# Kernel tuning notes

Hardware: AMD Instinct MI355X
Metric: run time of the kernel (lower is better)

The kernel has to match this reference:

```python
import jax, jax.numpy as jnp
import numpy as np

B, S, D, H, K = 16, 4096, 256, 512, 3
EPS = 1e-5


def setup_inputs() -> dict:
    key = jax.random.key(0)
    ks = jax.random.split(key, 16)
    glorot = lambda k, shape: jax.random.uniform(
        k, shape, jnp.float32, -1.0, 1.0) * np.sqrt(6.0 / (shape[0] + shape[-1]))
    return {
        "inputs": jax.random.normal(ks[0], (B, S, D), jnp.float32),
        "mask": jax.random.randint(ks[1], (B, S), 0, 2, jnp.int32),
        "in_w": glorot(ks[2], (H, D)),
        "in_b": jnp.zeros((H,), jnp.float32),
        "gate_w": glorot(ks[3], (H, D)),
        "gate_b": jnp.zeros((H,), jnp.float32),
        "dw_w": glorot(ks[4], (H, 1, K)),
        "dw_b": jnp.zeros((H,), jnp.float32),
        "pw_w": glorot(ks[5], (H, H, 1)),
        "pw_b": jnp.zeros((H,), jnp.float32),
        "ln_g": jnp.ones((H,), jnp.float32),
        "ln_b": jnp.zeros((H,), jnp.float32),
        "A_log": jax.random.normal(ks[6], (H,), jnp.float32) * -0.1,
        "Bp": jax.random.normal(ks[7], (H,), jnp.float32) * 0.1,
        "Cp": jax.random.normal(ks[8], (H,), jnp.float32) * 0.1,
    }


def _forward(inputs, mask, in_w, in_b, gate_w, gate_b, dw_w, dw_b,
             pw_w, pw_b, ln_g, ln_b, A_log, Bp, Cp):
    # projections: torch Linear is x @ W.T + b
    x_lin = jnp.einsum('bsd,hd->bsh', inputs, in_w) + in_b
    g_lin = jnp.einsum('bsd,hd->bsh', inputs, gate_w) + gate_b
    h = jnp.tanh(x_lin)
    m_f = mask.astype(h.dtype)                      # [B,S]
    h = h * m_f[:, :, None]
    # depthwise conv over time: [B,H,S] with groups=H, 'same' padding
    pad = (K - 1) // 2
    h_t = jnp.transpose(h, (0, 2, 1))               # [B,H,S]
    h_conv = jax.lax.conv_general_dilated(
        h_t, dw_w, window_strides=(1,), padding=[(pad, pad)],
        dimension_numbers=('NCH', 'OIH', 'NCH'), feature_group_count=H)
    h_conv = h_conv + dw_b[None, :, None]
    h_conv = jnp.transpose(h_conv, (0, 2, 1))       # [B,S,H]
    # pointwise 1x1 conv
    h_conv = jnp.einsum('bsh,oh->bso', h_conv, pw_w[:, :, 0]) + pw_b
    u = jax.nn.silu(h_conv + h)
    g = jax.nn.sigmoid(g_lin)
    a_exp = jnp.exp(-jax.nn.softplus(A_log))        # [H]

    def step(carry, xs):
        state, last = carry
        ut, gt, mt = xs                             # [B,H],[B,H],[B]
        new_state = gt * (a_exp * state) + (1.0 - gt) * (Bp * ut)
        keep = (mt > 0.5)[:, None]
        state = jnp.where(keep, new_state, state)
        y = state * Cp
        last = jnp.where(keep, y, last)
        return (state, last), last

    init = (jnp.zeros((B, H), u.dtype), jnp.zeros((B, H), u.dtype))
    xs = (jnp.transpose(u, (1, 0, 2)), jnp.transpose(g, (1, 0, 2)),
          jnp.transpose(m_f, (1, 0)))
    _, y_seq = jax.lax.scan(step, init, xs)         # [S,B,H]
    y_seq = jnp.transpose(y_seq, (1, 0, 2))         # [B,S,H]
    # LayerNorm over last dim
    mu = jnp.mean(y_seq, axis=-1, keepdims=True)
    var = jnp.var(y_seq, axis=-1, keepdims=True)
    return (y_seq - mu) * jax.lax.rsqrt(var + EPS) * ln_g + ln_b


def reference(inputs, mask, in_w, in_b, gate_w, gate_b, dw_w, dw_b,
              pw_w, pw_b, ln_g, ln_b, A_log, Bp, Cp):
    return _forward(inputs, mask, in_w, in_b, gate_w, gate_b, dw_w, dw_b,
                    pw_w, pw_b, ln_g, ln_b, A_log, Bp, Cp)
```

## Files before the change

kernel.cpp:

```cpp
#include <hip/hip_runtime.h>
#include <hip/hip_bf16.h>
#include <math.h>

#define B_  16
#define S_  4096
#define D_  256
#define H_  512
#define BS_ 65536
#define BSH_ 33554432L
#define BSD_ 16777216L
#define CCH 128
#define LCH 32
#define TPAD 136

typedef __bf16 bf16;
typedef __bf16 bf16x8 __attribute__((ext_vector_type(8)));
typedef float  f32x4  __attribute__((ext_vector_type(4)));

#define AS1 __attribute__((address_space(1)))
#define AS3 __attribute__((address_space(3)))

__device__ __forceinline__ void gload_lds16(const void* g, void* l) {
  __builtin_amdgcn_global_load_lds((const AS1 void*)g, (AS3 void*)l, 16, 0, 0);
}

#if __has_builtin(__builtin_amdgcn_exp2f)
#define EXP2F __builtin_amdgcn_exp2f
#else
#define EXP2F exp2f
#endif
#if __has_builtin(__builtin_amdgcn_rcpf)
#define RCPF __builtin_amdgcn_rcpf
#else
#define RCPF(x) (1.f/(x))
#endif
#define L2E 1.4426950408889634f

__device__ __forceinline__ float fsigmoid(float x) {
  return RCPF(1.f + EXP2F(-L2E * x));
}
__device__ __forceinline__ float ftanh(float x) {
  return 2.f * RCPF(1.f + EXP2F(-2.f * L2E * x)) - 1.f;
}
__device__ __forceinline__ float fsilu(float x) {
  return x * RCPF(1.f + EXP2F(-L2E * x));
}

__global__ void k_cast_x(const float* __restrict__ x, bf16* __restrict__ xb, int n8) {
  int i = blockIdx.x * blockDim.x + threadIdx.x;
  if (i >= n8) return;
  const float4* p = (const float4*)x + (long)i * 2;
  float4 a = p[0], b = p[1];
  bf16x8 o;
  o[0]=(bf16)a.x; o[1]=(bf16)a.y; o[2]=(bf16)a.z; o[3]=(bf16)a.w;
  o[4]=(bf16)b.x; o[5]=(bf16)b.y; o[6]=(bf16)b.z; o[7]=(bf16)b.w;
  ((bf16x8*)xb)[i] = o;
}

__global__ void k_cast_w(const float* __restrict__ in_w, const float* __restrict__ gate_w,
                         const float* __restrict__ pw_w,
                         bf16* __restrict__ w1, bf16* __restrict__ pw) {
  int i = blockIdx.x * blockDim.x + threadIdx.x;
  const int HD = H_ * D_;
  if (i < HD)            w1[i] = (bf16)in_w[i];
  else if (i < 2 * HD)   w1[i] = (bf16)gate_w[i - HD];
  else {
    int j = i - 2 * HD;
    if (j < H_ * H_)     pw[j] = (bf16)pw_w[j];
  }
}

template<int KDIM, int EPI>
__global__ __launch_bounds__(512, 5)
void k_gemm(const bf16* __restrict__ A, const bf16* __restrict__ Bw,
            const int* __restrict__ mask,
            const float* __restrict__ bias0, const float* __restrict__ bias1,
            const bf16* __restrict__ hbuf, const bf16* __restrict__ gbuf,
            const float* __restrict__ A_log, const float* __restrict__ Bp,
            float* __restrict__ Ac, float* __restrict__ Bc,
            bf16* __restrict__ out0, bf16* __restrict__ out1, int Ntiles)
{
  extern __shared__ char smem_raw[];
  bf16* tile = (bf16*)smem_raw;

  const int t = threadIdx.x;
  const int w = t >> 6, lane = t & 63;
  const int nwg = gridDim.x;
  const int wg = (blockIdx.x & 7) * (nwg >> 3) + (blockIdx.x >> 3);
  const int bn0 = (wg % Ntiles) * 128;
  const int bm0 = (wg / Ntiles) * 128;
  const int wm = w >> 2, wn = w & 3;
  const int fr = lane & 15, kq = lane >> 4;
  constexpr int NT = KDIM / 32;

  const bf16* Ag = A  + (long)(bm0 + (t >> 2)) * KDIM + (t & 3) * 8;
  const bf16* Bg = Bw + (long)(bn0 + (t >> 2)) * KDIM + (t & 3) * 8;

  f32x4 acc[4][2];
#pragma unroll
  for (int i = 0; i < 4; ++i)
#pragma unroll
    for (int j = 0; j < 2; ++j) acc[i][j] = (f32x4){0.f, 0.f, 0.f, 0.f};

#define STAGE(tt)                                                           \
  { char* _b = smem_raw + ((tt) & 1) * 16384;                               \
    gload_lds16(Ag + (tt) * 32, (bf16*)_b + t * 8);                         \
    gload_lds16(Bg + (tt) * 32, (bf16*)(_b + 8192) + t * 8); }

  STAGE(0); STAGE(1);

#pragma unroll
  for (int kt = 0; kt < NT; ++kt) {
    if (kt + 1 < NT) asm volatile("s_waitcnt vmcnt(2)" ::: "memory");
    else             asm volatile("s_waitcnt vmcnt(0)" ::: "memory");
    __builtin_amdgcn_s_barrier();

    const bf16* As = (const bf16*)(smem_raw + (kt & 1) * 16384);
    const bf16* Bs = As + 4096;
    bf16x8 af[4], bfr[2];
#pragma unroll
    for (int mi = 0; mi < 4; ++mi)
      af[mi] = *(const bf16x8*)&As[(wm * 64 + mi * 16 + fr) * 32 + kq * 8];
#pragma unroll
    for (int ni = 0; ni < 2; ++ni)
      bfr[ni] = *(const bf16x8*)&Bs[(wn * 32 + ni * 16 + fr) * 32 + kq * 8];

    asm volatile("s_waitcnt lgkmcnt(0)" ::: "memory");
    __builtin_amdgcn_s_barrier();

    if (kt + 2 < NT) STAGE(kt + 2);

#pragma unroll
    for (int mi = 0; mi < 4; ++mi)
#pragma unroll
      for (int ni = 0; ni < 2; ++ni)
        acc[mi][ni] = __builtin_amdgcn_mfma_f32_16x16x32_bf16(af[mi], bfr[ni], acc[mi][ni], 0, 0, 0);
  }
#undef STAGE

  __syncthreads();

  const bool hside = (EPI != 1) || (bn0 < H_);
#pragma unroll
  for (int mi = 0; mi < 4; ++mi) {
#pragma unroll
    for (int rr = 0; rr < 4; ++rr) {
      const int row = wm * 64 + mi * 16 + kq * 4 + rr;
      const int gm = bm0 + row;
      float mf = 1.f;
      if (EPI == 1) mf = (mask[gm] != 0) ? 1.f : 0.f;
#pragma unroll
      for (int ni = 0; ni < 2; ++ni) {
        const int col = wn * 32 + ni * 16 + fr;
        float c = acc[mi][ni][rr];
        float val;
        if (EPI == 1) {
          const int gn = bn0 + col;
          val = hside ? ftanh(c + bias0[gn]) * mf
                      : fsigmoid(c + bias1[gn - H_]);
        } else {
          val = c + bias0[bn0 + col];
        }
        tile[row * TPAD + col] = (bf16)val;
      }
    }
  }
  __syncthreads();

  const int pr = t >> 4;
  const int pc = (t & 15) * 8;
#pragma unroll
  for (int rr = 0; rr < 4; ++rr) {
    const int row = pr + rr * 32;
    const long gm = bm0 + row;
    bf16x8 v = *(const bf16x8*)&tile[row * TPAD + pc];
    if (EPI == 1) {
      if (hside) *(bf16x8*)&out0[gm * H_ + bn0 + pc] = v;
      else       *(bf16x8*)&out1[gm * H_ + (bn0 - H_) + pc] = v;
    } else {
      bf16x8 hb = *(const bf16x8*)&hbuf[gm * H_ + bn0 + pc];
      bf16x8 o;
#pragma unroll
      for (int k = 0; k < 8; ++k) {
        float s = (float)v[k] + (float)hb[k];
        o[k] = (bf16)fsilu(s);
      }
      *(bf16x8*)&out0[gm * H_ + bn0 + pc] = o;
      *(bf16x8*)&tile[row * TPAD + pc] = o;
    }
  }

  if constexpr (EPI == 2) {
    __syncthreads();
    const int c_idx = t >> 7;
    const int col   = t & 127;
    const int gcol  = bn0 + col;
    const int bIdx  = bm0 >> 12;
    const int s0    = bm0 & (S_ - 1);
    const int chunk = (s0 >> 5) + c_idx;
    const int* mrow = mask + bIdx * S_ + s0 + c_idx * 32;
    const float aexp = RCPF(1.f + EXP2F(L2E * A_log[gcol]));
    const float bp = Bp[gcol];
    const bf16* grow = gbuf + (long)(bm0 + c_idx * 32) * H_ + gcol;
    float At = 1.f, Bt = 0.f;
#pragma unroll 4
    for (int sl = 0; sl < LCH; ++sl) {
      float uv = (float)tile[(c_idx * 32 + sl) * TPAD + col];
      float gv = (float)grow[(long)sl * H_];
      bool mm = mrow[sl] != 0;
      float a_s = mm ? gv * aexp : 1.f;
      float b_s = mm ? (1.f - gv) * (bp * uv) : 0.f;
      At = a_s * At;
      Bt = fmaf(a_s, Bt, b_s);
    }
    long o = ((long)chunk * B_ + bIdx) * H_ + gcol;
    Ac[o] = At; Bc[o] = Bt;
  }
}

__global__ void k_dwconv(const bf16* __restrict__ h, const float* __restrict__ dww,
                         const float* __restrict__ dwb, bf16* __restrict__ hc)
{
  long idx = (long)blockIdx.x * blockDim.x + threadIdx.x;
  long m = idx >> 6;
  int h8 = ((int)idx & 63) << 3;
  int s = (int)(m & (S_ - 1));
  bf16x8 c0, c1, c2;
#pragma unroll
  for (int j = 0; j < 8; ++j) { c0[j] = (bf16)0.f; c2[j] = (bf16)0.f; }
  if (s > 0)        c0 = *(const bf16x8*)(h + (m - 1) * H_ + h8);
  c1 = *(const bf16x8*)(h + m * H_ + h8);
  if (s < S_ - 1)   c2 = *(const bf16x8*)(h + (m + 1) * H_ + h8);
  bf16x8 o;
#pragma unroll
  for (int j = 0; j < 8; ++j) {
    int hh = h8 + j;
    float v = (float)c0[j] * dww[hh * 3 + 0] + (float)c1[j] * dww[hh * 3 + 1]
            + (float)c2[j] * dww[hh * 3 + 2] + dwb[hh];
    o[j] = (bf16)v;
  }
  *(bf16x8*)(hc + m * H_ + h8) = o;
}


__global__ __launch_bounds__(256)
void k_scan2(const float* __restrict__ Ac, const float* __restrict__ Bc,
             float* __restrict__ Sin)
{
  int tid = blockIdx.x * 256 + threadIdx.x;
  int b = tid >> 9, h = tid & (H_ - 1);
  const long stride = (long)B_ * H_;
  long o = (long)b * H_ + h;
  float st = 0.f;
  float a = Ac[o], bb = Bc[o];
  for (int c = 0; c < CCH; ++c) {
    float an = 0.f, bn = 0.f;
    if (c + 1 < CCH) { an = Ac[o + stride]; bn = Bc[o + stride]; }
    Sin[o] = st;
    st = fmaf(a, st, bb);
    a = an; bb = bn; o += stride;
  }
}

__global__ __launch_bounds__(256)
void k_scan3(const bf16* __restrict__ u, const bf16* __restrict__ g,
             const int* __restrict__ mask, const float* __restrict__ A_log,
             const float* __restrict__ Bp, const float* __restrict__ Cp,
             const float* __restrict__ Sin,
             const float* __restrict__ ln_g, const float* __restrict__ ln_b,
             float* __restrict__ out)
{
  const int wv = threadIdx.x >> 6, lane = threadIdx.x & 63;
  const int c = blockIdx.x * 4 + wv;
  const int b = blockIdx.y;
  const int h0 = lane * 8;

  float aexp[8], bp[8], cp[8], lg[8], lb[8], st[8];
#pragma unroll
  for (int j = 0; j < 8; ++j) {
    aexp[j] = RCPF(1.f + EXP2F(L2E * A_log[h0 + j]));
    bp[j] = Bp[h0 + j]; cp[j] = Cp[h0 + j];
    lg[j] = ln_g[h0 + j]; lb[j] = ln_b[h0 + j];
    st[j] = Sin[((long)c * B_ + b) * H_ + h0 + j];
  }

  const long base = ((long)b * S_ + (long)c * LCH) * H_ + h0;
  const int* mrow = mask + b * S_ + c * LCH;

  bf16x8 uv = *(const bf16x8*)(u + base);
  bf16x8 gv = *(const bf16x8*)(g + base);
  int mm = mrow[0];

  for (int sl = 0; sl < LCH; ++sl) {
    bf16x8 un, gn; int mn = 0;
    if (sl + 1 < LCH) {
      un = *(const bf16x8*)(u + base + (long)(sl + 1) * H_);
      gn = *(const bf16x8*)(g + base + (long)(sl + 1) * H_);
      mn = mrow[sl + 1];
    }
    const bool m = mm != 0;
    float y[8], sum = 0.f, sq = 0.f;
#pragma unroll
    for (int j = 0; j < 8; ++j) {
      float uu = (float)uv[j], gg = (float)gv[j];
      float a_s = m ? gg * aexp[j] : 1.f;
      float b_s = m ? (1.f - gg) * (bp[j] * uu) : 0.f;
      st[j] = fmaf(a_s, st[j], b_s);
      y[j] = st[j] * cp[j];
      sum += y[j];
      sq = fmaf(y[j], y[j], sq);
    }
#pragma unroll
    for (int off = 32; off; off >>= 1) {
      sum += __shfl_xor(sum, off);
      sq  += __shfl_xor(sq, off);
    }
    const float mu = sum * (1.f / H_);
    const float var = sq * (1.f / H_) - mu * mu;
    const float rs = rsqrtf(var + 1e-5f);
    const long ob = base + (long)sl * H_;
    f32x4 o0, o1;
#pragma unroll
    for (int j = 0; j < 4; ++j) o0[j] = (y[j] - mu) * rs * lg[j] + lb[j];
#pragma unroll
    for (int j = 0; j < 4; ++j) o1[j] = (y[4 + j] - mu) * rs * lg[4 + j] + lb[4 + j];
    *(f32x4*)(out + ob) = o0;
    *(f32x4*)(out + ob + 4) = o1;
    uv = un; gv = gn; mm = mn;
  }
}

extern "C" void kernel_launch(void* const* d_in, const int* in_sizes, int n_in,
                              void* d_out, int out_size, void* d_ws, size_t ws_size,
                              hipStream_t stream)
{
  const float* x      = (const float*)d_in[0];
  const int*   mask   = (const int*)d_in[1];
  const float* in_w   = (const float*)d_in[2];
  const float* in_b   = (const float*)d_in[3];
  const float* gate_w = (const float*)d_in[4];
  const float* gate_b = (const float*)d_in[5];
  const float* dw_w   = (const float*)d_in[6];
  const float* dw_b   = (const float*)d_in[7];
  const float* pw_w   = (const float*)d_in[8];
  const float* pw_b   = (const float*)d_in[9];
  const float* ln_g   = (const float*)d_in[10];
  const float* ln_b   = (const float*)d_in[11];
  const float* A_log  = (const float*)d_in[12];
  const float* Bp     = (const float*)d_in[13];
  const float* Cp     = (const float*)d_in[14];

  char* ws = (char*)d_ws;
  bf16*  xb  = (bf16*)(ws + 0L);
  bf16*  h   = (bf16*)(ws + 33554432L);
  bf16*  hc  = (bf16*)(ws + 100663296L);
  bf16*  u   = (bf16*)(ws + 167772160L);
  bf16*  g   = (bf16*)(ws + 234881024L);
  bf16*  w1  = (bf16*)(ws + 301989888L);
  bf16*  pw  = (bf16*)(ws + 302514176L);
  float* Ac  = (float*)(ws + 303038464L);
  float* Bc  = (float*)(ws + 307232768L);
  float* Sin = (float*)(ws + 311427072L);
  float* out = (float*)d_out;

  const int gemm_lds = 128 * TPAD * 2;

  k_cast_x<<<8192, 256, 0, stream>>>(x, xb, (int)(BSD_ / 8));
  k_cast_w<<<2048, 256, 0, stream>>>(in_w, gate_w, pw_w, w1, pw);
  k_gemm<256, 1><<<512 * 8, 512, gemm_lds, stream>>>(
      xb, w1, mask, in_b, gate_b, nullptr, nullptr, nullptr, nullptr,
      nullptr, nullptr, h, g, 8);
  k_dwconv<<<16384, 256, 0, stream>>>(h, dw_w, dw_b, hc);
  k_gemm<512, 2><<<512 * 4, 512, gemm_lds, stream>>>(
      hc, pw, mask, pw_b, nullptr, h, g, A_log, Bp,
      Ac, Bc, u, nullptr, 4);
  k_scan2<<<32, 256, 0, stream>>>(Ac, Bc, Sin);
  k_scan3<<<dim3(CCH / 4, B_), 256, 0, stream>>>(
      u, g, mask, A_log, Bp, Cp, Sin, ln_g, ln_b, out);
}
```

Before: 326.4 us.

## Fuse input cast into GEMM1 and depthwise conv into GEMM2 A-loads

Removes the separate fp32-to-bf16 input cast kernel: GEMM1 now reads fp32 activations, converts them in registers and writes them into LDS. It also removes the standalone depthwise-conv kernel: GEMM2 computes the 3-tap conv on the fly from h (three rows per stage, weights staged in LDS) while building its A tiles. This cuts two kernel launches and the global round trips for xb and hc. In exchange, the async global-to-LDS A path gives way to register-staged loads with a plain single-barrier double buffer, which exposes more load latency. The conv inputs are also re-read once per N tile, and occupancy is lowered to 4.

Measured after the change: 347.7 us. 1.07x slower.

```diff
diff --git a/kernel.cpp b/kernel.cpp
--- a/kernel.cpp
+++ b/kernel.cpp
@@ -7,8 +7,6 @@
 #define D_  256
 #define H_  512
 #define BS_ 65536
-#define BSH_ 33554432L
-#define BSD_ 16777216L
 #define CCH 128
 #define LCH 32
 #define TPAD 136
@@ -46,17 +44,6 @@
   return x * RCPF(1.f + EXP2F(-L2E * x));
 }
 
-__global__ void k_cast_x(const float* __restrict__ x, bf16* __restrict__ xb, int n8) {
-  int i = blockIdx.x * blockDim.x + threadIdx.x;
-  if (i >= n8) return;
-  const float4* p = (const float4*)x + (long)i * 2;
-  float4 a = p[0], b = p[1];
-  bf16x8 o;
-  o[0]=(bf16)a.x; o[1]=(bf16)a.y; o[2]=(bf16)a.z; o[3]=(bf16)a.w;
-  o[4]=(bf16)b.x; o[5]=(bf16)b.y; o[6]=(bf16)b.z; o[7]=(bf16)b.w;
-  ((bf16x8*)xb)[i] = o;
-}
-
 __global__ void k_cast_w(const float* __restrict__ in_w, const float* __restrict__ gate_w,
                          const float* __restrict__ pw_w,
                          bf16* __restrict__ w1, bf16* __restrict__ pw) {
@@ -70,19 +57,14 @@
   }
 }
 
-template<int KDIM, int EPI>
-__global__ __launch_bounds__(512, 5)
-void k_gemm(const bf16* __restrict__ A, const bf16* __restrict__ Bw,
-            const int* __restrict__ mask,
-            const float* __restrict__ bias0, const float* __restrict__ bias1,
-            const bf16* __restrict__ hbuf, const bf16* __restrict__ gbuf,
-            const float* __restrict__ A_log, const float* __restrict__ Bp,
-            float* __restrict__ Ac, float* __restrict__ Bc,
-            bf16* __restrict__ out0, bf16* __restrict__ out1, int Ntiles)
+__global__ __launch_bounds__(512, 4)
+void k_gemm1(const float* __restrict__ X, const bf16* __restrict__ Bw,
+             const int* __restrict__ mask,
+             const float* __restrict__ bias0, const float* __restrict__ bias1,
+             bf16* __restrict__ out0, bf16* __restrict__ out1, int Ntiles)
 {
-  extern __shared__ char smem_raw[];
-  bf16* tile = (bf16*)smem_raw;
-
+  extern __shared__ char smem[];
+  bf16* tile = (bf16*)smem;
   const int t = threadIdx.x;
   const int w = t >> 6, lane = t & 63;
   const int nwg = gridDim.x;
@@ -91,10 +73,10 @@
   const int bm0 = (wg / Ntiles) * 128;
   const int wm = w >> 2, wn = w & 3;
   const int fr = lane & 15, kq = lane >> 4;
-  constexpr int NT = KDIM / 32;
-
-  const bf16* Ag = A  + (long)(bm0 + (t >> 2)) * KDIM + (t & 3) * 8;
-  const bf16* Bg = Bw + (long)(bn0 + (t >> 2)) * KDIM + (t & 3) * 8;
+  constexpr int KDIM = 256, NT = 8;
+
+  const float* Xg = X + (long)(bm0 + (t >> 2)) * KDIM + (t & 3) * 8;
+  const bf16*  Bg = Bw + (long)(bn0 + (t >> 2)) * KDIM + (t & 3) * 8;
 
   f32x4 acc[4][2];
 #pragma unroll
@@ -102,20 +84,22 @@
 #pragma unroll
     for (int j = 0; j < 2; ++j) acc[i][j] = (f32x4){0.f, 0.f, 0.f, 0.f};
 
-#define STAGE(tt)                                                           \
-  { char* _b = smem_raw + ((tt) & 1) * 16384;                               \
-    gload_lds16(Ag + (tt) * 32, (bf16*)_b + t * 8);                         \
-    gload_lds16(Bg + (tt) * 32, (bf16*)(_b + 8192) + t * 8); }
-
-  STAGE(0); STAGE(1);
-
+#define STAGE1(tt)                                                          \
+  { const int _bi = (tt) & 1;                                               \
+    f32x4 xa = *(const f32x4*)(Xg + (tt) * 32);                             \
+    f32x4 xb = *(const f32x4*)(Xg + (tt) * 32 + 4);                         \
+    bf16x8 av;                                                              \
+    _Pragma("unroll")                                                       \
+    for (int j = 0; j < 4; ++j) { av[j] = (bf16)xa[j]; av[4+j] = (bf16)xb[j]; } \
+    *(bf16x8*)((bf16*)(smem + _bi * 16384) + t * 8) = av;                   \
+    gload_lds16(Bg + (tt) * 32, (bf16*)(smem + _bi * 16384 + 8192) + t * 8); }
+
+  STAGE1(0);
 #pragma unroll
   for (int kt = 0; kt < NT; ++kt) {
-    if (kt + 1 < NT) asm volatile("s_waitcnt vmcnt(2)" ::: "memory");
-    else             asm volatile("s_waitcnt vmcnt(0)" ::: "memory");
-    __builtin_amdgcn_s_barrier();
-
-    const bf16* As = (const bf16*)(smem_raw + (kt & 1) * 16384);
+    __syncthreads();
+    if (kt + 1 < NT) STAGE1(kt + 1);
+    const bf16* As = (const bf16*)(smem + (kt & 1) * 16384);
     const bf16* Bs = As + 4096;
     bf16x8 af[4], bfr[2];
 #pragma unroll
@@ -124,43 +108,31 @@
 #pragma unroll
     for (int ni = 0; ni < 2; ++ni)
       bfr[ni] = *(const bf16x8*)&Bs[(wn * 32 + ni * 16 + fr) * 32 + kq * 8];
-
-    asm volatile("s_waitcnt lgkmcnt(0)" ::: "memory");
-    __builtin_amdgcn_s_barrier();
-
-    if (kt + 2 < NT) STAGE(kt + 2);
-
 #pragma unroll
     for (int mi = 0; mi < 4; ++mi)
 #pragma unroll
       for (int ni = 0; ni < 2; ++ni)
         acc[mi][ni] = __builtin_amdgcn_mfma_f32_16x16x32_bf16(af[mi], bfr[ni], acc[mi][ni], 0, 0, 0);
   }
-#undef STAGE
-
-  __syncthreads();
-
-  const bool hside = (EPI != 1) || (bn0 < H_);
+#undef STAGE1
+
+  __syncthreads();
+
+  const bool hside = (bn0 < H_);
 #pragma unroll
   for (int mi = 0; mi < 4; ++mi) {
 #pragma unroll
     for (int rr = 0; rr < 4; ++rr) {
       const int row = wm * 64 + mi * 16 + kq * 4 + rr;
       const int gm = bm0 + row;
-      float mf = 1.f;
-      if (EPI == 1) mf = (mask[gm] != 0) ? 1.f : 0.f;
+      const float mf = (mask[gm] != 0) ? 1.f : 0.f;
 #pragma unroll
       for (int ni = 0; ni < 2; ++ni) {
         const int col = wn * 32 + ni * 16 + fr;
-        float c = acc[mi][ni][rr];
-        float val;
-        if (EPI == 1) {
-          const int gn = bn0 + col;
-          val = hside ? ftanh(c + bias0[gn]) * mf
-                      : fsigmoid(c + bias1[gn - H_]);
-        } else {
-          val = c + bias0[bn0 + col];
-        }
+        const int gn = bn0 + col;
+        const float c = acc[mi][ni][rr];
+        const float val = hside ? ftanh(c + bias0[gn]) * mf
+                                : fsigmoid(c + bias1[gn - H_]);
         tile[row * TPAD + col] = (bf16)val;
       }
     }
@@ -174,74 +146,154 @@
     const int row = pr + rr * 32;
     const long gm = bm0 + row;
     bf16x8 v = *(const bf16x8*)&tile[row * TPAD + pc];
-    if (EPI == 1) {
-      if (hside) *(bf16x8*)&out0[gm * H_ + bn0 + pc] = v;
-      else       *(bf16x8*)&out1[gm * H_ + (bn0 - H_) + pc] = v;
-    } else {
-      bf16x8 hb = *(const bf16x8*)&hbuf[gm * H_ + bn0 + pc];
-      bf16x8 o;
-#pragma unroll
-      for (int k = 0; k < 8; ++k) {
-        float s = (float)v[k] + (float)hb[k];
-        o[k] = (bf16)fsilu(s);
+    if (hside) *(bf16x8*)&out0[gm * H_ + bn0 + pc] = v;
+    else       *(bf16x8*)&out1[gm * H_ + (bn0 - H_) + pc] = v;
+  }
+}
+
+__global__ __launch_bounds__(512, 4)
+void k_gemm2(const bf16* __restrict__ h, const bf16* __restrict__ Bw,
+             const int* __restrict__ mask, const float* __restrict__ pwb,
+             const float* __restrict__ dww, const float* __restrict__ dwb,
+             const bf16* __restrict__ gbuf, const float* __restrict__ A_log,
+             const float* __restrict__ Bp,
+             float* __restrict__ Ac, float* __restrict__ Bc,
+             bf16* __restrict__ u, int Ntiles)
+{
+  extern __shared__ char smem[];
+  bf16* tile = (bf16*)smem;
+  float* wt = (float*)(smem + 34816);
+  float* wb = wt + 1536;
+  const int t = threadIdx.x;
+  const int w = t >> 6, lane = t & 63;
+  const int nwg = gridDim.x;
+  const int wg = (blockIdx.x & 7) * (nwg >> 3) + (blockIdx.x >> 3);
+  const int bn0 = (wg % Ntiles) * 128;
+  const int bm0 = (wg / Ntiles) * 128;
+  const int wm = w >> 2, wn = w & 3;
+  const int fr = lane & 15, kq = lane >> 4;
+  constexpr int KDIM = 512, NT = 16;
+
+  for (int i = t; i < 1536; i += 512) wt[i] = dww[(i & 511) * 3 + (i >> 9)];
+  if (t < 512) wb[t] = dwb[t];
+
+  const int sr = t >> 2, sc8 = (t & 3) * 8;
+  const long gm = bm0 + sr;
+  const int s = (int)(gm & (S_ - 1));
+  const bool has_m = (s > 0), has_p = (s < S_ - 1);
+  const bf16* hp = h + gm * (long)H_ + sc8;
+  const bf16* Bg = Bw + (long)(bn0 + sr) * KDIM + sc8;
+
+  f32x4 acc[4][2];
+#pragma unroll
+  for (int i = 0; i < 4; ++i)
+#pragma unroll
+    for (int j = 0; j < 2; ++j) acc[i][j] = (f32x4){0.f, 0.f, 0.f, 0.f};
+
+  __syncthreads();
+
+#define STAGE2(tt)                                                          \
+  { const int _bi = (tt) & 1;                                               \
+    const int ch = (tt) * 32 + sc8;                                         \
+    bf16x8 a0, a1, a2;                                                      \
+    _Pragma("unroll")                                                       \
+    for (int j = 0; j < 8; ++j) { a0[j] = (bf16)0.f; a2[j] = (bf16)0.f; }   \
+    a1 = *(const bf16x8*)(hp + (tt) * 32);                                  \
+    if (has_m) a0 = *(const bf16x8*)(hp + (tt) * 32 - H_);                  \
+    if (has_p) a2 = *(const bf16x8*)(hp + (tt) * 32 + H_);                  \
+    f32x4 w0a = *(const f32x4*)(wt + ch),        w0b = *(const f32x4*)(wt + ch + 4); \
+    f32x4 w1a = *(const f32x4*)(wt + 512 + ch),  w1b = *(const f32x4*)(wt + 512 + ch + 4); \
+    f32x4 w2a = *(const f32x4*)(wt + 1024 + ch), w2b = *(const f32x4*)(wt + 1024 + ch + 4); \
+    f32x4 ba  = *(const f32x4*)(wb + ch),        bb  = *(const f32x4*)(wb + ch + 4); \
+    bf16x8 o;                                                               \
+    _Pragma("unroll")                                                       \
+    for (int j = 0; j < 4; ++j) {                                           \
+      o[j]   = (bf16)((float)a0[j]   * w0a[j] + (float)a1[j]   * w1a[j]     \
+                    + (float)a2[j]   * w2a[j] + ba[j]);                     \
+      o[4+j] = (bf16)((float)a0[4+j] * w0b[j] + (float)a1[4+j] * w1b[j]     \
+                    + (float)a2[4+j] * w2b[j] + bb[j]);                     \
+    }                                                                       \
+    *(bf16x8*)((bf16*)(smem + _bi * 16384) + t * 8) = o;                    \
+    gload_lds16(Bg + (tt) * 32, (bf16*)(smem + _bi * 16384 + 8192) + t * 8); }
+
+  STAGE2(0);
+#pragma unroll
+  for (int kt = 0; kt < NT; ++kt) {
+    __syncthreads();
+    if (kt + 1 < NT) STAGE2(kt + 1);
+    const bf16* As = (const bf16*)(smem + (kt & 1) * 16384);
+    const bf16* Bs = As + 4096;
+    bf16x8 af[4], bfr[2];
+#pragma unroll
+    for (int mi = 0; mi < 4; ++mi)
+      af[mi] = *(const bf16x8*)&As[(wm * 64 + mi * 16 + fr) * 32 + kq * 8];
+#pragma unroll
+    for (int ni = 0; ni < 2; ++ni)
+      bfr[ni] = *(const bf16x8*)&Bs[(wn * 32 + ni * 16 + fr) * 32 + kq * 8];
+#pragma unroll
+    for (int mi = 0; mi < 4; ++mi)
+#pragma unroll
+      for (int ni = 0; ni < 2; ++ni)
+        acc[mi][ni] = __builtin_amdgcn_mfma_f32_16x16x32_bf16(af[mi], bfr[ni], acc[mi][ni], 0, 0, 0);
+  }
+#undef STAGE2
+
+  __syncthreads();
+
+#pragma unroll
+  for (int mi = 0; mi < 4; ++mi) {
+#pragma unroll
+    for (int rr = 0; rr < 4; ++rr) {
+      const int row = wm * 64 + mi * 16 + kq * 4 + rr;
+#pragma unroll
+      for (int ni = 0; ni < 2; ++ni) {
+        const int col = wn * 32 + ni * 16 + fr;
+        tile[row * TPAD + col] = (bf16)(acc[mi][ni][rr] + pwb[bn0 + col]);
       }
-      *(bf16x8*)&out0[gm * H_ + bn0 + pc] = o;
-      *(bf16x8*)&tile[row * TPAD + pc] = o;
     }
   }
-
-  if constexpr (EPI == 2) {
-    __syncthreads();
-    const int c_idx = t >> 7;
-    const int col   = t & 127;
-    const int gcol  = bn0 + col;
-    const int bIdx  = bm0 >> 12;
-    const int s0    = bm0 & (S_ - 1);
-    const int chunk = (s0 >> 5) + c_idx;
-    const int* mrow = mask + bIdx * S_ + s0 + c_idx * 32;
-    const float aexp = RCPF(1.f + EXP2F(L2E * A_log[gcol]));
-    const float bp = Bp[gcol];
-    const bf16* grow = gbuf + (long)(bm0 + c_idx * 32) * H_ + gcol;
-    float At = 1.f, Bt = 0.f;
+  __syncthreads();
+
+  const int pr = t >> 4;
+  const int pc = (t & 15) * 8;
+#pragma unroll
+  for (int rr = 0; rr < 4; ++rr) {
+    const int row = pr + rr * 32;
+    const long gmr = bm0 + row;
+    bf16x8 v = *(const bf16x8*)&tile[row * TPAD + pc];
+    bf16x8 hb = *(const bf16x8*)&h[gmr * H_ + bn0 + pc];
+    bf16x8 o;
+#pragma unroll
+    for (int k = 0; k < 8; ++k) o[k] = (bf16)fsilu((float)v[k] + (float)hb[k]);
+    *(bf16x8*)&u[gmr * H_ + bn0 + pc] = o;
+    *(bf16x8*)&tile[row * TPAD + pc] = o;
+  }
+
+  __syncthreads();
+  const int c_idx = t >> 7;
+  const int col   = t & 127;
+  const int gcol  = bn0 + col;
+  const int bIdx  = bm0 >> 12;
+  const int s0    = bm0 & (S_ - 1);
+  const int chunk = (s0 >> 5) + c_idx;
+  const int* mrow = mask + bIdx * S_ + s0 + c_idx * 32;
+  const float aexp = RCPF(1.f + EXP2F(L2E * A_log[gcol]));
+  const float bp = Bp[gcol];
+  const bf16* grow = gbuf + (long)(bm0 + c_idx * 32) * H_ + gcol;
+  float At = 1.f, Bt = 0.f;
 #pragma unroll 4
-    for (int sl = 0; sl < LCH; ++sl) {
-      float uv = (float)tile[(c_idx * 32 + sl) * TPAD + col];
-      float gv = (float)grow[(long)sl * H_];
-      bool mm = mrow[sl] != 0;
-      float a_s = mm ? gv * aexp : 1.f;
-      float b_s = mm ? (1.f - gv) * (bp * uv) : 0.f;
-      At = a_s * At;
-      Bt = fmaf(a_s, Bt, b_s);
-    }
-    long o = ((long)chunk * B_ + bIdx) * H_ + gcol;
-    Ac[o] = At; Bc[o] = Bt;
-  }
-}
-
-__global__ void k_dwconv(const bf16* __restrict__ h, const float* __restrict__ dww,
-                         const float* __restrict__ dwb, bf16* __restrict__ hc)
-{
-  long idx = (long)blockIdx.x * blockDim.x + threadIdx.x;
-  long m = idx >> 6;
-  int h8 = ((int)idx & 63) << 3;
-  int s = (int)(m & (S_ - 1));
-  bf16x8 c0, c1, c2;
-#pragma unroll
-  for (int j = 0; j < 8; ++j) { c0[j] = (bf16)0.f; c2[j] = (bf16)0.f; }
-  if (s > 0)        c0 = *(const bf16x8*)(h + (m - 1) * H_ + h8);
-  c1 = *(const bf16x8*)(h + m * H_ + h8);
-  if (s < S_ - 1)   c2 = *(const bf16x8*)(h + (m + 1) * H_ + h8);
-  bf16x8 o;
-#pragma unroll
-  for (int j = 0; j < 8; ++j) {
-    int hh = h8 + j;
-    float v = (float)c0[j] * dww[hh * 3 + 0] + (float)c1[j] * dww[hh * 3 + 1]
-            + (float)c2[j] * dww[hh * 3 + 2] + dwb[hh];
-    o[j] = (bf16)v;
-  }
-  *(bf16x8*)(hc + m * H_ + h8) = o;
-}
-
+  for (int sl = 0; sl < LCH; ++sl) {
+    float uv = (float)tile[(c_idx * 32 + sl) * TPAD + col];
+    float gv = (float)grow[(long)sl * H_];
+    bool mm = mrow[sl] != 0;
+    float a_s = mm ? gv * aexp : 1.f;
+    float b_s = mm ? (1.f - gv) * (bp * uv) : 0.f;
+    At = a_s * At;
+    Bt = fmaf(a_s, Bt, b_s);
+  }
+  long o = ((long)chunk * B_ + bIdx) * H_ + gcol;
+  Ac[o] = At; Bc[o] = Bt;
+}
 
 __global__ __launch_bounds__(256)
 void k_scan2(const float* __restrict__ Ac, const float* __restrict__ Bc,
@@ -351,9 +403,7 @@
   const float* Cp     = (const float*)d_in[14];
 
   char* ws = (char*)d_ws;
-  bf16*  xb  = (bf16*)(ws + 0L);
   bf16*  h   = (bf16*)(ws + 33554432L);
-  bf16*  hc  = (bf16*)(ws + 100663296L);
   bf16*  u   = (bf16*)(ws + 167772160L);
   bf16*  g   = (bf16*)(ws + 234881024L);
   bf16*  w1  = (bf16*)(ws + 301989888L);
@@ -363,17 +413,15 @@
   float* Sin = (float*)(ws + 311427072L);
   float* out = (float*)d_out;
 
-  const int gemm_lds = 128 * TPAD * 2;
-
-  k_cast_x<<<8192, 256, 0, stream>>>(x, xb, (int)(BSD_ / 8));
   k_cast_w<<<2048, 256, 0, stream>>>(in_w, gate_w, pw_w, w1, pw);
-  k_gemm<256, 1><<<512 * 8, 512, gemm_lds, stream>>>(
-      xb, w1, mask, in_b, gate_b, nullptr, nullptr, nullptr, nullptr,
-      nullptr, nullptr, h, g, 8);
-  k_dwconv<<<16384, 256, 0, stream>>>(h, dw_w, dw_b, hc);
-  k_gemm<512, 2><<<512 * 4, 512, gemm_lds, stream>>>(
-      hc, pw, mask, pw_b, nullptr, h, g, A_log, Bp,
-      Ac, Bc, u, nullptr, 4);
+
+  k_gemm1<<<512 * 8, 512, 34816, stream>>>(
+      x, w1, mask, in_b, gate_b, h, g, 8);
+
+  k_gemm2<<<512 * 4, 512, 43008, stream>>>(
+      h, pw, mask, pw_b, dw_w, dw_b, g, A_log, Bp,
+      Ac, Bc, u, 4);
+
   k_scan2<<<32, 256, 0, stream>>>(Ac, Bc, Sin);
   k_scan3<<<dim3(CCH / 4, B_), 256, 0, stream>>>(
       u, g, mask, A_log, Bp, Cp, Sin, ln_g, ln_b, out);
```
